# Optimization experiments

Hardware: AMD Instinct MI355X
Metric: run time of the kernel (lower is better)

The kernel has to match this reference:

```python
import jax, jax.numpy as jnp
import numpy as np

B, T, DIN, H, NOUT = 256, 512, 64, 512, 128


def setup_inputs() -> dict:
    key = jax.random.key(0)
    ks = jax.random.split(key, 11)
    s = 1.0 / np.sqrt(H)  # PyTorch GRU init scale
    inp = {"x": jax.random.normal(ks[0], (B, T, DIN), dtype=jnp.float32)}
    # layer 0 (input DIN), layer 1 (input H); gate order: r, z, n
    inp["w_ih0"] = jax.random.uniform(ks[1], (3 * H, DIN), minval=-s, maxval=s)
    inp["w_hh0"] = jax.random.uniform(ks[2], (3 * H, H), minval=-s, maxval=s)
    inp["b_ih0"] = jax.random.uniform(ks[3], (3 * H,), minval=-s, maxval=s)
    inp["b_hh0"] = jax.random.uniform(ks[4], (3 * H,), minval=-s, maxval=s)
    inp["w_ih1"] = jax.random.uniform(ks[5], (3 * H, H), minval=-s, maxval=s)
    inp["w_hh1"] = jax.random.uniform(ks[6], (3 * H, H), minval=-s, maxval=s)
    inp["b_ih1"] = jax.random.uniform(ks[7], (3 * H,), minval=-s, maxval=s)
    inp["b_hh1"] = jax.random.uniform(ks[8], (3 * H,), minval=-s, maxval=s)
    inp["w_fc"] = jax.random.uniform(ks[9], (NOUT, H), minval=-s, maxval=s)
    inp["b_fc"] = jax.random.uniform(ks[10], (NOUT,), minval=-s, maxval=s)
    return inp


def _gru_layer(x_seq, w_ih, w_hh, b_ih, b_hh):
    # x_seq: [B, T, Din] -> hidden trajectory [B, T, H]
    xg = jnp.einsum('btd,gd->btg', x_seq, w_ih) + b_ih  # [B, T, 3H], precomputed input gates
    h0 = jnp.zeros((x_seq.shape[0], w_hh.shape[1]), dtype=x_seq.dtype)

    def step(h, xg_t):
        hg = h @ w_hh.T + b_hh
        xr, xz, xn = jnp.split(xg_t, 3, axis=-1)
        hr, hz, hn = jnp.split(hg, 3, axis=-1)
        r = jax.nn.sigmoid(xr + hr)
        z = jax.nn.sigmoid(xz + hz)
        n = jnp.tanh(xn + r * hn)
        h_new = (1.0 - z) * n + z * h
        return h_new, h_new

    _, hs = jax.lax.scan(step, h0, jnp.swapaxes(xg, 0, 1))  # [T, B, H]
    return jnp.swapaxes(hs, 0, 1)


def reference(x, w_ih0, w_hh0, b_ih0, b_hh0, w_ih1, w_hh1, b_ih1, b_hh1, w_fc, b_fc):
    h1 = _gru_layer(x, w_ih0, w_hh0, b_ih0, b_hh0)   # [B, T, H]
    h2 = _gru_layer(h1, w_ih1, w_hh1, b_ih1, b_hh1)  # [B, T, H]
    last = h2[:, -1, :]                               # [B, H]
    return last @ w_fc.T + b_fc                       # [B, NOUT]
```

## Files before the change

kernel.cpp:

```cpp
#include <hip/hip_runtime.h>
#include <math.h>

typedef unsigned short u16;
typedef __attribute__((ext_vector_type(8))) short s8v;
typedef __attribute__((ext_vector_type(4))) float f4v;
typedef __attribute__((ext_vector_type(4))) int   i4v;

constexpr int kB    = 256;
constexpr int kT    = 512;
constexpr int kDIN  = 64;
constexpr int kH    = 512;
constexpr int kG3   = 1536;
constexpr int kNOUT = 128;
constexpr int kPlane = 8 * 2 * 16 * 512;

__device__ __forceinline__ u16 f2bf(float f) {
  union { float f; unsigned u; } v; v.f = f;
  unsigned r = (v.u + 0x7FFFu + ((v.u >> 16) & 1u)) >> 16;
  return (u16)r;
}
__device__ __forceinline__ float fsig(float x) {
  x = fminf(fmaxf(x, -30.f), 30.f);
  float e = __expf(-x);
  return __fdividef(1.f, 1.f + e);
}
__device__ __forceinline__ float ftanh(float x) {
  x = fminf(fmaxf(x, -15.f), 15.f);
  float e = __expf(-2.f * x);
  return __fdividef(1.f - e, 1.f + e);
}

__device__ __forceinline__ void load_afrag16(const u16* base, i4v a[16]) {
  asm volatile(
      "global_load_dwordx4 %0, %16, off sc0 sc1\n\t"
      "global_load_dwordx4 %1, %16, off offset:1024 sc0 sc1\n\t"
      "global_load_dwordx4 %2, %16, off offset:2048 sc0 sc1\n\t"
      "global_load_dwordx4 %3, %16, off offset:3072 sc0 sc1\n\t"
      "global_load_dwordx4 %4, %17, off sc0 sc1\n\t"
      "global_load_dwordx4 %5, %17, off offset:1024 sc0 sc1\n\t"
      "global_load_dwordx4 %6, %17, off offset:2048 sc0 sc1\n\t"
      "global_load_dwordx4 %7, %17, off offset:3072 sc0 sc1\n\t"
      "global_load_dwordx4 %8, %18, off sc0 sc1\n\t"
      "global_load_dwordx4 %9, %18, off offset:1024 sc0 sc1\n\t"
      "global_load_dwordx4 %10, %18, off offset:2048 sc0 sc1\n\t"
      "global_load_dwordx4 %11, %18, off offset:3072 sc0 sc1\n\t"
      "global_load_dwordx4 %12, %19, off sc0 sc1\n\t"
      "global_load_dwordx4 %13, %19, off offset:1024 sc0 sc1\n\t"
      "global_load_dwordx4 %14, %19, off offset:2048 sc0 sc1\n\t"
      "global_load_dwordx4 %15, %19, off offset:3072 sc0 sc1\n\t"
      "s_waitcnt vmcnt(0)"
      : "=&v"(a[0]), "=&v"(a[1]), "=&v"(a[2]), "=&v"(a[3]),
        "=&v"(a[4]), "=&v"(a[5]), "=&v"(a[6]), "=&v"(a[7]),
        "=&v"(a[8]), "=&v"(a[9]), "=&v"(a[10]), "=&v"(a[11]),
        "=&v"(a[12]), "=&v"(a[13]), "=&v"(a[14]), "=&v"(a[15])
      : "v"(base), "v"(base + 4 * 512), "v"(base + 8 * 512), "v"(base + 12 * 512)
      : "memory");
}

__device__ __forceinline__ void store_h_l0(
    u16* p0, u16* p1, u16* p2, u16* p3,
    u16* q0, u16* q1, u16* q2, u16* q3,
    unsigned v0, unsigned v1, unsigned v2, unsigned v3) {
  asm volatile(
      "global_store_short %0, %8, off sc0 sc1\n\t"
      "global_store_short %1, %9, off sc0 sc1\n\t"
      "global_store_short %2, %10, off sc0 sc1\n\t"
      "global_store_short %3, %11, off sc0 sc1\n\t"
      "global_store_short %4, %8, off\n\t"
      "global_store_short %5, %9, off\n\t"
      "global_store_short %6, %10, off\n\t"
      "global_store_short %7, %11, off\n\t"
      "s_waitcnt vmcnt(4)"
      :: "v"(p0), "v"(p1), "v"(p2), "v"(p3),
         "v"(q0), "v"(q1), "v"(q2), "v"(q3),
         "v"(v0), "v"(v1), "v"(v2), "v"(v3)
      : "memory");
}
__device__ __forceinline__ void store_h_l1(
    u16* p0, u16* p1, u16* p2, u16* p3,
    unsigned v0, unsigned v1, unsigned v2, unsigned v3) {
  asm volatile(
      "global_store_short %0, %4, off sc0 sc1\n\t"
      "global_store_short %1, %5, off sc0 sc1\n\t"
      "global_store_short %2, %6, off sc0 sc1\n\t"
      "global_store_short %3, %7, off sc0 sc1\n\t"
      "s_waitcnt vmcnt(0)"
      :: "v"(p0), "v"(p1), "v"(p2), "v"(p3),
         "v"(v0), "v"(v1), "v"(v2), "v"(v3)
      : "memory");
}

__global__ void build_wslab(const float* __restrict__ w, u16* __restrict__ d) {
  int idx  = blockIdx.x * 256 + threadIdx.x;
  int lane = idx & 63, fg = idx >> 6;
  int jt = fg / 96, f = fg % 96;
  int nt = f >> 4, kt = f & 15;
  int g = nt >> 1, u = nt & 1;
  int row = g * 512 + jt * 32 + u * 16 + (lane & 15);
  int k0  = kt * 32 + (lane >> 4) * 8;
  const float* src = w + (size_t)row * 512 + k0;
  u16* dst = d + ((size_t)fg) * 512 + lane * 8;
#pragma unroll
  for (int i = 0; i < 8; i++) dst[i] = f2bf(src[i]);
}

__global__ __launch_bounds__(256, 1)
void coop_rec(int c, int TC, int nc, unsigned bar_base16, unsigned* bar,
              const float* __restrict__ xg0, const float* __restrict__ xg1,
              const u16* __restrict__ wslab0, const u16* __restrict__ wslab1,
              const float* __restrict__ bhh0, const float* __restrict__ bhh1,
              u16* __restrict__ h1seq, u16* __restrict__ hbuf,
              float* __restrict__ carry) {
  const int bid   = blockIdx.x;
  const int layer = bid >> 7;
  const int lb    = bid & 127;
  const int jt    = lb & 15, bt = lb >> 4;
  const int cc    = (layer == 0) ? c : c - 1;
  const bool active = (cc >= 0 && cc < nc);

  unsigned* mybar = bar + (size_t)(layer * 8 + bt) * 64;

  if (!active) {
    if (threadIdx.x == 0)
      __hip_atomic_fetch_add(mybar, (unsigned)TC, __ATOMIC_RELAXED,
                             __HIP_MEMORY_SCOPE_AGENT);
    return;
  }

  const float* xg    = layer ? xg1 : xg0;
  const u16*  wslab  = layer ? wslab1 : wslab0;
  const float* bhh   = layer ? bhh1 : bhh0;
  float* mycarry = carry + (size_t)layer * kB * kH;

  const int tid  = threadIdx.x;
  const int wv   = tid >> 6, lane = tid & 63;
  const int mt   = wv >> 1, u = wv & 1;
  const int b0   = bt * 32;
  const int jl   = lane & 15;
  const int jg   = jt * 32 + u * 16 + jl;
  const int mrow = (lane >> 4) * 4;

  s8v bfr[3][16];
  {
    const u16* base = wslab + (size_t)jt * 96 * 512;
#pragma unroll
    for (int g = 0; g < 3; ++g)
#pragma unroll
      for (int kt = 0; kt < 16; ++kt)
        bfr[g][kt] = *(const s8v*)&base[(size_t)((g * 2 + u) * 16 + kt) * 512 + lane * 8];
  }
  const float bh_r = bhh[jg], bh_z = bhh[512 + jg], bh_n = bhh[1024 + jg];

  float hp[4];
#pragma unroll
  for (int r = 0; r < 4; ++r)
    hp[r] = mycarry[(size_t)(b0 + mt * 16 + mrow + r) * 512 + jg];

  const size_t cons_off = ((size_t)((bt * 2 + mt) * 16)) * 512 + lane * 8;
  const size_t prod_off = ((size_t)((bt * 2 + mt) * 16 + jt)) * 512 +
                          (size_t)(16 * (u * 2 + (jl >> 3))) * 8 + (jl & 7);
  const int bbase = b0 + mt * 16 + mrow;

  float xv0[4], xv1[4], xv2[4];
  auto prefetch_xg = [&](int tt) {
#pragma unroll
    for (int r = 0; r < 4; ++r) {
      const float* xp = xg + ((size_t)(bbase + r) * TC + tt) * kG3;
      xv0[r] = xp[jg]; xv1[r] = xp[512 + jg]; xv2[r] = xp[1024 + jg];
    }
  };
  prefetch_xg(0);

  for (int t = 0; t < TC; ++t) {
    if (tid == 0) {
      unsigned tgt = bar_base16 + 16u * (unsigned)t;
      int guard = 0;
      while (__hip_atomic_load(mybar, __ATOMIC_RELAXED,
                               __HIP_MEMORY_SCOPE_AGENT) < tgt
             && ++guard < (1 << 21)) {
        __builtin_amdgcn_s_sleep(1);
      }
    }
    __syncthreads();

    const u16* plane = hbuf + (size_t)(layer * 2 + (t & 1)) * kPlane;
    i4v a[16];
    load_afrag16(plane + cons_off, a);

    f4v acc0 = {0.f, 0.f, 0.f, 0.f}, acc1 = acc0, acc2 = acc0;
#pragma unroll
    for (int kt = 0; kt < 16; ++kt) {
      const s8v av = __builtin_bit_cast(s8v, a[kt]);
      acc0 = __builtin_amdgcn_mfma_f32_16x16x32_bf16(av, bfr[0][kt], acc0, 0, 0, 0);
      acc1 = __builtin_amdgcn_mfma_f32_16x16x32_bf16(av, bfr[1][kt], acc1, 0, 0, 0);
      acc2 = __builtin_amdgcn_mfma_f32_16x16x32_bf16(av, bfr[2][kt], acc2, 0, 0, 0);
    }

    unsigned hv[4];
#pragma unroll
    for (int r = 0; r < 4; ++r) {
      float rr = fsig(xv0[r] + acc0[r] + bh_r);
      float zz = fsig(xv1[r] + acc1[r] + bh_z);
      float nn = ftanh(xv2[r] + rr * (acc2[r] + bh_n));
      float hn = (1.f - zz) * nn + zz * hp[r];
      hp[r] = hn;
      hv[r] = f2bf(hn);
    }

    u16* pb = hbuf + (size_t)(layer * 2 + ((t + 1) & 1)) * kPlane + prod_off;
    if (layer == 0) {
      u16* q = h1seq + ((size_t)bbase * TC + t) * 512 + jg;
      store_h_l0(pb + (size_t)(mrow + 0) * 8, pb + (size_t)(mrow + 1) * 8,
                 pb + (size_t)(mrow + 2) * 8, pb + (size_t)(mrow + 3) * 8,
                 q, q + (size_t)TC * 512, q + 2 * (size_t)TC * 512,
                 q + 3 * (size_t)TC * 512,
                 hv[0], hv[1], hv[2], hv[3]);
    } else {
      store_h_l1(pb + (size_t)(mrow + 0) * 8, pb + (size_t)(mrow + 1) * 8,
                 pb + (size_t)(mrow + 2) * 8, pb + (size_t)(mrow + 3) * 8,
                 hv[0], hv[1], hv[2], hv[3]);
    }
    __syncthreads();
    if (tid == 0)
      __hip_atomic_fetch_add(mybar, 1u, __ATOMIC_RELAXED,
                             __HIP_MEMORY_SCOPE_AGENT);
    if (t + 1 < TC) prefetch_xg(t + 1);
  }

#pragma unroll
  for (int r = 0; r < 4; ++r)
    mycarry[(size_t)(bbase + r) * 512 + jg] = hp[r];
}

__device__ void gemm_role(int idx, int TC,
                          const float* __restrict__ Af, const u16* __restrict__ Ab,
                          int Abstride, int Atoff, int K,
                          const float* __restrict__ Bf, const float* __restrict__ bias,
                          float* __restrict__ C, char* smem) {
  u16* As = (u16*)smem;
  u16* Bs = As + 128 * 40;
  const int tid = threadIdx.x;
  const int mt = idx / 12, nt = idx % 12;
  const int m0 = mt * 128, n0 = nt * 128;
  const int w = tid >> 6, lane = tid & 63;
  const int wm = w & 1, wn = w >> 1;
  const int ra = tid >> 2, koff = (tid & 3) * 8;

  const int r = m0 + ra;
  const size_t aoff = ((size_t)(r / TC) * Abstride + Atoff + (r % TC)) * K;
  const float* arowF = Af ? Af + aoff : nullptr;
  const u16*  arowB = Ab ? Ab + aoff : nullptr;
  const float* browF = Bf + (size_t)(n0 + ra) * K;

  f4v acc[4][2];
#pragma unroll
  for (int i = 0; i < 4; i++)
#pragma unroll
    for (int jn = 0; jn < 2; jn++) acc[i][jn] = (f4v){0.f, 0.f, 0.f, 0.f};

  for (int k0 = 0; k0 < K; k0 += 32) {
    s8v av, bv;
    if (arowB) {
      av = *(const s8v*)(arowB + k0 + koff);
    } else {
      u16 tmp[8];
      const float* ap = arowF + k0 + koff;
#pragma unroll
      for (int i = 0; i < 8; i++) tmp[i] = f2bf(ap[i]);
      av = *(s8v*)tmp;
    }
    {
      u16 tmp[8];
      const float* bp = browF + k0 + koff;
#pragma unroll
      for (int i = 0; i < 8; i++) tmp[i] = f2bf(bp[i]);
      bv = *(s8v*)tmp;
    }
    __syncthreads();
    *(s8v*)&As[ra * 40 + koff] = av;
    *(s8v*)&Bs[ra * 40 + koff] = bv;
    __syncthreads();
    s8v af[4];
#pragma unroll
    for (int i = 0; i < 4; i++)
      af[i] = *(const s8v*)&As[(wm * 64 + i * 16 + (lane & 15)) * 40 + (lane >> 4) * 8];
#pragma unroll
    for (int jn = 0; jn < 2; jn++) {
      s8v bf = *(const s8v*)&Bs[(wn * 32 + jn * 16 + (lane & 15)) * 40 + (lane >> 4) * 8];
#pragma unroll
      for (int i = 0; i < 4; i++)
        acc[i][jn] = __builtin_amdgcn_mfma_f32_16x16x32_bf16(af[i], bf, acc[i][jn], 0, 0, 0);
    }
  }

#pragma unroll
  for (int jn = 0; jn < 2; jn++) {
    int n = n0 + wn * 32 + jn * 16 + (lane & 15);
    float bv2 = bias[n];
#pragma unroll
    for (int i = 0; i < 4; i++) {
      int mrow = m0 + wm * 64 + i * 16 + (lane >> 4) * 4;
#pragma unroll
      for (int reg = 0; reg < 4; reg++)
        C[(size_t)(mrow + reg) * kG3 + n] = acc[i][jn][reg] + bv2;
    }
  }
}

__global__ __launch_bounds__(512)
void gemm_kernel(int TC, const float* Af, const u16* Ab, int Abstride, int Atoff,
                 int K, const float* Bf, const float* bias, float* C) {
  __shared__ __align__(16) char smem[2 * 128 * 40 * 2];
  gemm_role(blockIdx.x, TC, Af, Ab, Abstride, Atoff, K, Bf, bias, C, smem);
}

__global__ __launch_bounds__(512)
void gemm2_kernel(int TC, int G1, int do0,
                  const float* x, int atoff0, const u16* h1seq,
                  const float* wih0, const float* bih0, float* xg0,
                  const float* wih1, const float* bih1, float* xg1) {
  __shared__ __align__(16) char smem[2 * 128 * 40 * 2];
  if ((int)blockIdx.x < G1) {
    gemm_role(blockIdx.x, TC, nullptr, h1seq, TC, 0, kH, wih1, bih1, xg1, smem);
  } else if (do0) {
    gemm_role(blockIdx.x - G1, TC, x, nullptr, kT, atoff0, kDIN, wih0, bih0,
              xg0, smem);
  }
}

__global__ __launch_bounds__(128)
void fc_kernel(const float* __restrict__ h, const float* __restrict__ wfc,
               const float* __restrict__ bfc, float* __restrict__ out) {
  const int b = blockIdx.x;
  const int n = threadIdx.x;
  const float* hrow = h + (size_t)b * kH;
  const float* wrow = wfc + (size_t)n * kH;
  float acc = 0.f;
#pragma unroll 4
  for (int k = 0; k < kH; k += 4) {
    const float4 hv = *(const float4*)&hrow[k];
    const float4 wv = *(const float4*)&wrow[k];
    acc = fmaf(hv.x, wv.x, acc); acc = fmaf(hv.y, wv.y, acc);
    acc = fmaf(hv.z, wv.z, acc); acc = fmaf(hv.w, wv.w, acc);
  }
  out[(size_t)b * kNOUT + n] = acc + bfc[n];
}

extern "C" void kernel_launch(void* const* d_in, const int* in_sizes, int n_in,
                              void* d_out, int out_size, void* d_ws, size_t ws_size,
                              hipStream_t stream) {
  const float* x     = (const float*)d_in[0];
  const float* w_ih0 = (const float*)d_in[1];
  const float* w_hh0 = (const float*)d_in[2];
  const float* b_ih0 = (const float*)d_in[3];
  const float* b_hh0 = (const float*)d_in[4];
  const float* w_ih1 = (const float*)d_in[5];
  const float* w_hh1 = (const float*)d_in[6];
  const float* b_ih1 = (const float*)d_in[7];
  const float* b_hh1 = (const float*)d_in[8];
  const float* w_fc  = (const float*)d_in[9];
  const float* b_fc  = (const float*)d_in[10];
  float* out = (float*)d_out;

  auto need = [](int tc) -> size_t {
    size_t s = 0;
    s += 2 * (size_t)kB * tc * kG3 * 4;
    s += (size_t)kB * tc * kH * 2;
    s += 2 * (size_t)kG3 * kH * 2;
    s += 4 * (size_t)kPlane * 2;
    s += 2 * (size_t)kB * kH * 4;
    s += 32768;
    return s;
  };
  int TC = 64;
  while (TC > 2 && need(TC) > ws_size) TC >>= 1;
  const int nc = kT / TC;

  char* p = (char*)d_ws;
  auto carve = [&](size_t bytes) {
    char* r = p; p += (bytes + 255) & ~(size_t)255; return r;
  };
  float* xg0   = (float*)carve((size_t)kB * TC * kG3 * 4);
  float* xg1   = (float*)carve((size_t)kB * TC * kG3 * 4);
  u16* h1seq   = (u16*)carve((size_t)kB * TC * kH * 2);
  u16* wslab0  = (u16*)carve((size_t)kG3 * kH * 2);
  u16* wslab1  = (u16*)carve((size_t)kG3 * kH * 2);
  u16* hbuf    = (u16*)carve(4 * (size_t)kPlane * 2);
  float* carry = (float*)carve(2 * (size_t)kB * kH * 4);
  unsigned* bar = (unsigned*)carve(32 * 64 * sizeof(unsigned));

  build_wslab<<<384, 256, 0, stream>>>(w_hh0, wslab0);
  build_wslab<<<384, 256, 0, stream>>>(w_hh1, wslab1);
  hipMemsetAsync(hbuf, 0, 4 * (size_t)kPlane * 2 + 2 * (size_t)kB * kH * 4, stream);
  hipMemsetAsync(bar, 0, 32 * 64 * sizeof(unsigned), stream);

  const int G1 = 24 * TC;

  gemm_kernel<<<dim3(G1), 512, 0, stream>>>(TC, x, nullptr, kT, 0, kDIN,
                                            w_ih0, b_ih0, xg0);

  for (int c = 0; c <= nc; ++c) {
    unsigned base16 = (unsigned)c * 16u * (unsigned)TC;
    coop_rec<<<dim3(256), dim3(256), 0, stream>>>(
        c, TC, nc, base16, bar, xg0, xg1, wslab0, wslab1,
        b_hh0, b_hh1, h1seq, hbuf, carry);
    if (c < nc) {
      int do0 = (c + 1 < nc) ? 1 : 0;
      gemm2_kernel<<<dim3(2 * G1), 512, 0, stream>>>(
          TC, G1, do0, x, (c + 1) * TC, h1seq,
          w_ih0, b_ih0, xg0, w_ih1, b_ih1, xg1);
    }
  }

  fc_kernel<<<dim3(kB), dim3(kNOUT), 0, stream>>>(
      carry + (size_t)kB * kH, w_fc, b_fc, out);
}
```

Before: 2.586 ms.

## Fuse input-gate GEMMs into recurrent kernel with double-buffered chunk pipeline

Merges the per-chunk input-projection GEMM launches into the recurrent kernel as extra blocks. It double-buffers xg and h1 so that layer-1 recurrence runs two chunks behind layer 0, and the GEMM for chunk c-1 (layer 1) and c+1 (layer 0) runs alongside the recurrence. The GEMM is reworked to 256 threads with a 4x4 MFMA tile per wave, and TC is halved to 32 so the double buffers fit. This aims to remove the serial gap between GEMM and recurrence launches. In exchange it adds more launches, one extra pipeline stage and contention between GEMM blocks and the persistent recurrent blocks.

```diff
diff --git a/kernel.cpp b/kernel.cpp
--- a/kernel.cpp
+++ b/kernel.cpp
@@ -104,18 +104,124 @@
   for (int i = 0; i < 8; i++) dst[i] = f2bf(src[i]);
 }
 
+__device__ void gemm_role256(int idx, int TC,
+                             const float* __restrict__ Af, const u16* __restrict__ Ab,
+                             int Abstride, int Atoff, int K,
+                             const float* __restrict__ Bf, const float* __restrict__ bias,
+                             float* __restrict__ C, char* smem) {
+  u16* As = (u16*)smem;
+  u16* Bs = As + 128 * 40;
+  const int tid = threadIdx.x;
+  const int mt = idx / 12, nt = idx % 12;
+  const int m0 = mt * 128, n0 = nt * 128;
+  const int w = tid >> 6, lane = tid & 63;
+  const int wm = w & 1, wn = w >> 1;
+  const int ra = tid >> 1, koff = (tid & 1) * 16;
+
+  const int r = m0 + ra;
+  const size_t aoff = ((size_t)(r / TC) * Abstride + Atoff + (r % TC)) * K;
+  const float* arowF = Af ? Af + aoff : nullptr;
+  const u16*  arowB = Ab ? Ab + aoff : nullptr;
+  const float* browF = Bf + (size_t)(n0 + ra) * K;
+
+  f4v acc[4][4];
+#pragma unroll
+  for (int i = 0; i < 4; i++)
+#pragma unroll
+    for (int j = 0; j < 4; j++) acc[i][j] = (f4v){0.f, 0.f, 0.f, 0.f};
+
+  for (int k0 = 0; k0 < K; k0 += 32) {
+    s8v av0, av1, bv0, bv1;
+    if (arowB) {
+      av0 = *(const s8v*)(arowB + k0 + koff);
+      av1 = *(const s8v*)(arowB + k0 + koff + 8);
+    } else {
+      u16 t0[8], t1[8];
+      const float* ap = arowF + k0 + koff;
+#pragma unroll
+      for (int i = 0; i < 8; i++) { t0[i] = f2bf(ap[i]); t1[i] = f2bf(ap[8 + i]); }
+      av0 = *(s8v*)t0; av1 = *(s8v*)t1;
+    }
+    {
+      u16 t0[8], t1[8];
+      const float* bp = browF + k0 + koff;
+#pragma unroll
+      for (int i = 0; i < 8; i++) { t0[i] = f2bf(bp[i]); t1[i] = f2bf(bp[8 + i]); }
+      bv0 = *(s8v*)t0; bv1 = *(s8v*)t1;
+    }
+    __syncthreads();
+    *(s8v*)&As[ra * 40 + koff]     = av0;
+    *(s8v*)&As[ra * 40 + koff + 8] = av1;
+    *(s8v*)&Bs[ra * 40 + koff]     = bv0;
+    *(s8v*)&Bs[ra * 40 + koff + 8] = bv1;
+    __syncthreads();
+    s8v af[4], bf[4];
+#pragma unroll
+    for (int i = 0; i < 4; i++)
+      af[i] = *(const s8v*)&As[(wm * 64 + i * 16 + (lane & 15)) * 40 + (lane >> 4) * 8];
+#pragma unroll
+    for (int j = 0; j < 4; j++)
+      bf[j] = *(const s8v*)&Bs[(wn * 64 + j * 16 + (lane & 15)) * 40 + (lane >> 4) * 8];
+#pragma unroll
+    for (int j = 0; j < 4; j++)
+#pragma unroll
+      for (int i = 0; i < 4; i++)
+        acc[i][j] = __builtin_amdgcn_mfma_f32_16x16x32_bf16(af[i], bf[j], acc[i][j], 0, 0, 0);
+  }
+
+#pragma unroll
+  for (int j = 0; j < 4; j++) {
+    int n = n0 + wn * 64 + j * 16 + (lane & 15);
+    float bv2 = bias[n];
+#pragma unroll
+    for (int i = 0; i < 4; i++) {
+      int mrow = m0 + wm * 64 + i * 16 + (lane >> 4) * 4;
+#pragma unroll
+      for (int reg = 0; reg < 4; reg++)
+        C[(size_t)(mrow + reg) * kG3 + n] = acc[i][j][reg] + bv2;
+    }
+  }
+}
+
 __global__ __launch_bounds__(256, 1)
-void coop_rec(int c, int TC, int nc, unsigned bar_base16, unsigned* bar,
-              const float* __restrict__ xg0, const float* __restrict__ xg1,
-              const u16* __restrict__ wslab0, const u16* __restrict__ wslab1,
-              const float* __restrict__ bhh0, const float* __restrict__ bhh1,
-              u16* __restrict__ h1seq, u16* __restrict__ hbuf,
-              float* __restrict__ carry) {
-  const int bid   = blockIdx.x;
+void fused_rec(int c, int TC, int nc, int G1, unsigned bar_base16,
+               unsigned* bar,
+               const float* __restrict__ x,
+               const float* __restrict__ xg0a, const float* __restrict__ xg0b,
+               const float* __restrict__ xg1a, const float* __restrict__ xg1b,
+               u16* __restrict__ h1a, u16* __restrict__ h1b,
+               const u16* __restrict__ wslab0, const u16* __restrict__ wslab1,
+               const float* __restrict__ bhh0, const float* __restrict__ bhh1,
+               const float* __restrict__ wih0, const float* __restrict__ bih0,
+               const float* __restrict__ wih1, const float* __restrict__ bih1,
+               u16* __restrict__ hbuf, float* __restrict__ carry) {
+  const int bid = blockIdx.x;
+
+  if (bid >= 256) {
+    __shared__ __align__(16) char smem[2 * 128 * 40 * 2];
+    int g = bid - 256;
+    if (g < G1) {
+      int cp = c - 1;
+      if (cp >= 0 && cp < nc) {
+        const u16* A = (cp & 1) ? h1b : h1a;
+        float* O = (float*)((cp & 1) ? xg1b : xg1a);
+        gemm_role256(g, TC, nullptr, A, TC, 0, kH, wih1, bih1, O, smem);
+      }
+    } else {
+      int cn = c + 1;
+      if (cn < nc) {
+        float* O = (float*)((cn & 1) ? xg0b : xg0a);
+        gemm_role256(g - G1, TC, x, nullptr, kT, cn * TC, kDIN, wih0, bih0,
+                     O, smem);
+      }
+    }
+    return;
+  }
+
   const int layer = bid >> 7;
   const int lb    = bid & 127;
   const int jt    = lb & 15, bt = lb >> 4;
-  const int cc    = (layer == 0) ? c : c - 1;
+  const int cc    = (layer == 0) ? c : c - 2;
   const bool active = (cc >= 0 && cc < nc);
 
   unsigned* mybar = bar + (size_t)(layer * 8 + bt) * 64;
@@ -127,9 +233,11 @@
     return;
   }
 
-  const float* xg    = layer ? xg1 : xg0;
-  const u16*  wslab  = layer ? wslab1 : wslab0;
-  const float* bhh   = layer ? bhh1 : bhh0;
+  const float* xg   = layer ? ((cc & 1) ? xg1b : xg1a)
+                            : ((cc & 1) ? xg0b : xg0a);
+  u16* h1seq        = (cc & 1) ? h1b : h1a;
+  const u16*  wslab = layer ? wslab1 : wslab0;
+  const float* bhh  = layer ? bhh1 : bhh0;
   float* mycarry = carry + (size_t)layer * kB * kH;
 
   const int tid  = threadIdx.x;
@@ -232,100 +340,12 @@
     mycarry[(size_t)(bbase + r) * 512 + jg] = hp[r];
 }
 
-__device__ void gemm_role(int idx, int TC,
-                          const float* __restrict__ Af, const u16* __restrict__ Ab,
-                          int Abstride, int Atoff, int K,
-                          const float* __restrict__ Bf, const float* __restrict__ bias,
-                          float* __restrict__ C, char* smem) {
-  u16* As = (u16*)smem;
-  u16* Bs = As + 128 * 40;
-  const int tid = threadIdx.x;
-  const int mt = idx / 12, nt = idx % 12;
-  const int m0 = mt * 128, n0 = nt * 128;
-  const int w = tid >> 6, lane = tid & 63;
-  const int wm = w & 1, wn = w >> 1;
-  const int ra = tid >> 2, koff = (tid & 3) * 8;
-
-  const int r = m0 + ra;
-  const size_t aoff = ((size_t)(r / TC) * Abstride + Atoff + (r % TC)) * K;
-  const float* arowF = Af ? Af + aoff : nullptr;
-  const u16*  arowB = Ab ? Ab + aoff : nullptr;
-  const float* browF = Bf + (size_t)(n0 + ra) * K;
-
-  f4v acc[4][2];
-#pragma unroll
-  for (int i = 0; i < 4; i++)
-#pragma unroll
-    for (int jn = 0; jn < 2; jn++) acc[i][jn] = (f4v){0.f, 0.f, 0.f, 0.f};
-
-  for (int k0 = 0; k0 < K; k0 += 32) {
-    s8v av, bv;
-    if (arowB) {
-      av = *(const s8v*)(arowB + k0 + koff);
-    } else {
-      u16 tmp[8];
-      const float* ap = arowF + k0 + koff;
-#pragma unroll
-      for (int i = 0; i < 8; i++) tmp[i] = f2bf(ap[i]);
-      av = *(s8v*)tmp;
-    }
-    {
-      u16 tmp[8];
-      const float* bp = browF + k0 + koff;
-#pragma unroll
-      for (int i = 0; i < 8; i++) tmp[i] = f2bf(bp[i]);
-      bv = *(s8v*)tmp;
-    }
-    __syncthreads();
-    *(s8v*)&As[ra * 40 + koff] = av;
-    *(s8v*)&Bs[ra * 40 + koff] = bv;
-    __syncthreads();
-    s8v af[4];
-#pragma unroll
-    for (int i = 0; i < 4; i++)
-      af[i] = *(const s8v*)&As[(wm * 64 + i * 16 + (lane & 15)) * 40 + (lane >> 4) * 8];
-#pragma unroll
-    for (int jn = 0; jn < 2; jn++) {
-      s8v bf = *(const s8v*)&Bs[(wn * 32 + jn * 16 + (lane & 15)) * 40 + (lane >> 4) * 8];
-#pragma unroll
-      for (int i = 0; i < 4; i++)
-        acc[i][jn] = __builtin_amdgcn_mfma_f32_16x16x32_bf16(af[i], bf, acc[i][jn], 0, 0, 0);
-    }
-  }
-
-#pragma unroll
-  for (int jn = 0; jn < 2; jn++) {
-    int n = n0 + wn * 32 + jn * 16 + (lane & 15);
-    float bv2 = bias[n];
-#pragma unroll
-    for (int i = 0; i < 4; i++) {
-      int mrow = m0 + wm * 64 + i * 16 + (lane >> 4) * 4;
-#pragma unroll
-      for (int reg = 0; reg < 4; reg++)
-        C[(size_t)(mrow + reg) * kG3 + n] = acc[i][jn][reg] + bv2;
-    }
-  }
-}
-
-__global__ __launch_bounds__(512)
-void gemm_kernel(int TC, const float* Af, const u16* Ab, int Abstride, int Atoff,
-                 int K, const float* Bf, const float* bias, float* C) {
+__global__ __launch_bounds__(256)
+void gemm_kernel256(int TC, const float* Af, const u16* Ab, int Abstride,
+                    int Atoff, int K, const float* Bf, const float* bias,
+                    float* C) {
   __shared__ __align__(16) char smem[2 * 128 * 40 * 2];
-  gemm_role(blockIdx.x, TC, Af, Ab, Abstride, Atoff, K, Bf, bias, C, smem);
-}
-
-__global__ __launch_bounds__(512)
-void gemm2_kernel(int TC, int G1, int do0,
-                  const float* x, int atoff0, const u16* h1seq,
-                  const float* wih0, const float* bih0, float* xg0,
-                  const float* wih1, const float* bih1, float* xg1) {
-  __shared__ __align__(16) char smem[2 * 128 * 40 * 2];
-  if ((int)blockIdx.x < G1) {
-    gemm_role(blockIdx.x, TC, nullptr, h1seq, TC, 0, kH, wih1, bih1, xg1, smem);
-  } else if (do0) {
-    gemm_role(blockIdx.x - G1, TC, x, nullptr, kT, atoff0, kDIN, wih0, bih0,
-              xg0, smem);
-  }
+  gemm_role256(blockIdx.x, TC, Af, Ab, Abstride, Atoff, K, Bf, bias, C, smem);
 }
 
 __global__ __launch_bounds__(128)
@@ -364,15 +384,15 @@
 
   auto need = [](int tc) -> size_t {
     size_t s = 0;
-    s += 2 * (size_t)kB * tc * kG3 * 4;
-    s += (size_t)kB * tc * kH * 2;
+    s += 4 * (size_t)kB * tc * kG3 * 4;
+    s += 2 * (size_t)kB * tc * kH * 2;
     s += 2 * (size_t)kG3 * kH * 2;
     s += 4 * (size_t)kPlane * 2;
     s += 2 * (size_t)kB * kH * 4;
-    s += 32768;
+    s += 65536;
     return s;
   };
-  int TC = 64;
+  int TC = 32;
   while (TC > 2 && need(TC) > ws_size) TC >>= 1;
   const int nc = kT / TC;
 
@@ -380,9 +400,12 @@
   auto carve = [&](size_t bytes) {
     char* r = p; p += (bytes + 255) & ~(size_t)255; return r;
   };
-  float* xg0   = (float*)carve((size_t)kB * TC * kG3 * 4);
-  float* xg1   = (float*)carve((size_t)kB * TC * kG3 * 4);
-  u16* h1seq   = (u16*)carve((size_t)kB * TC * kH * 2);
+  float* xg0a  = (float*)carve((size_t)kB * TC * kG3 * 4);
+  float* xg0b  = (float*)carve((size_t)kB * TC * kG3 * 4);
+  float* xg1a  = (float*)carve((size_t)kB * TC * kG3 * 4);
+  float* xg1b  = (float*)carve((size_t)kB * TC * kG3 * 4);
+  u16* h1a     = (u16*)carve((size_t)kB * TC * kH * 2);
+  u16* h1b     = (u16*)carve((size_t)kB * TC * kH * 2);
   u16* wslab0  = (u16*)carve((size_t)kG3 * kH * 2);
   u16* wslab1  = (u16*)carve((size_t)kG3 * kH * 2);
   u16* hbuf    = (u16*)carve(4 * (size_t)kPlane * 2);
@@ -396,20 +419,17 @@
 
   const int G1 = 24 * TC;
 
-  gemm_kernel<<<dim3(G1), 512, 0, stream>>>(TC, x, nullptr, kT, 0, kDIN,
-                                            w_ih0, b_ih0, xg0);
-
-  for (int c = 0; c <= nc; ++c) {
+  gemm_kernel256<<<dim3(G1), 256, 0, stream>>>(TC, x, nullptr, kT, 0, kDIN,
+                                               w_ih0, b_ih0, xg0a);
+
+  for (int c = 0; c <= nc + 1; ++c) {
     unsigned base16 = (unsigned)c * 16u * (unsigned)TC;
-    coop_rec<<<dim3(256), dim3(256), 0, stream>>>(
-        c, TC, nc, base16, bar, xg0, xg1, wslab0, wslab1,
-        b_hh0, b_hh1, h1seq, hbuf, carry);
-    if (c < nc) {
-      int do0 = (c + 1 < nc) ? 1 : 0;
-      gemm2_kernel<<<dim3(2 * G1), 512, 0, stream>>>(
-          TC, G1, do0, x, (c + 1) * TC, h1seq,
-          w_ih0, b_ih0, xg0, w_ih1, b_ih1, xg1);
-    }
+    fused_rec<<<dim3(256 + 2 * G1), dim3(256), 0, stream>>>(
+        c, TC, nc, G1, base16, bar, x,
+        xg0a, xg0b, xg1a, xg1b, h1a, h1b,
+        wslab0, wslab1, b_hh0, b_hh1,
+        w_ih0, b_ih0, w_ih1, b_ih1,
+        hbuf, carry);
   }
 
   fc_kernel<<<dim3(kB), dim3(kNOUT), 0, stream>>>(
```

New measurement: 3.066 ms. 1.19x slower.

## Fuse input projections into a single persistent wavefront-pipelined two-layer GRU kernel

Applied to the files above, without the earlier changes.

Removes the chunked launches of the recurrent kernel and the separate input-gate GEMM kernels. Both layers now run in one persistent kernel: layer 0 computes its input projection in-loop from a pre-packed bf16 x plane, and layer 1 computes its input projection from layer 0's live hidden state. Per-layer counters form a skewed wavefront so layer 1 runs one step behind layer 0. The goal is to drop the fp32 xg round trips through memory, the h1seq staging and the per-chunk launch and sync overhead. The cost is extra MFMA work in the serial step path, and layer 1 now streams its input weights from global memory every step.

```diff
diff --git a/kernel.cpp b/kernel.cpp
--- a/kernel.cpp
+++ b/kernel.cpp
@@ -13,6 +13,9 @@
 constexpr int kG3   = 1536;
 constexpr int kNOUT = 128;
 constexpr int kPlane = 8 * 2 * 16 * 512;
+constexpr int kXStep = 16 * 2 * 512;
+
+#define MFMA16 __builtin_amdgcn_mfma_f32_16x16x32_bf16
 
 __device__ __forceinline__ u16 f2bf(float f) {
   union { float f; unsigned u; } v; v.f = f;
@@ -56,27 +59,59 @@
       : "v"(base), "v"(base + 4 * 512), "v"(base + 8 * 512), "v"(base + 12 * 512)
       : "memory");
 }
-
-__device__ __forceinline__ void store_h_l0(
-    u16* p0, u16* p1, u16* p2, u16* p3,
-    u16* q0, u16* q1, u16* q2, u16* q3,
-    unsigned v0, unsigned v1, unsigned v2, unsigned v3) {
+__device__ __forceinline__ void load16_nw(const u16* base, i4v a[16]) {
   asm volatile(
-      "global_store_short %0, %8, off sc0 sc1\n\t"
-      "global_store_short %1, %9, off sc0 sc1\n\t"
-      "global_store_short %2, %10, off sc0 sc1\n\t"
-      "global_store_short %3, %11, off sc0 sc1\n\t"
-      "global_store_short %4, %8, off\n\t"
-      "global_store_short %5, %9, off\n\t"
-      "global_store_short %6, %10, off\n\t"
-      "global_store_short %7, %11, off\n\t"
-      "s_waitcnt vmcnt(4)"
-      :: "v"(p0), "v"(p1), "v"(p2), "v"(p3),
-         "v"(q0), "v"(q1), "v"(q2), "v"(q3),
-         "v"(v0), "v"(v1), "v"(v2), "v"(v3)
+      "global_load_dwordx4 %0, %16, off sc0 sc1\n\t"
+      "global_load_dwordx4 %1, %16, off offset:1024 sc0 sc1\n\t"
+      "global_load_dwordx4 %2, %16, off offset:2048 sc0 sc1\n\t"
+      "global_load_dwordx4 %3, %16, off offset:3072 sc0 sc1\n\t"
+      "global_load_dwordx4 %4, %17, off sc0 sc1\n\t"
+      "global_load_dwordx4 %5, %17, off offset:1024 sc0 sc1\n\t"
+      "global_load_dwordx4 %6, %17, off offset:2048 sc0 sc1\n\t"
+      "global_load_dwordx4 %7, %17, off offset:3072 sc0 sc1\n\t"
+      "global_load_dwordx4 %8, %18, off sc0 sc1\n\t"
+      "global_load_dwordx4 %9, %18, off offset:1024 sc0 sc1\n\t"
+      "global_load_dwordx4 %10, %18, off offset:2048 sc0 sc1\n\t"
+      "global_load_dwordx4 %11, %18, off offset:3072 sc0 sc1\n\t"
+      "global_load_dwordx4 %12, %19, off sc0 sc1\n\t"
+      "global_load_dwordx4 %13, %19, off offset:1024 sc0 sc1\n\t"
+      "global_load_dwordx4 %14, %19, off offset:2048 sc0 sc1\n\t"
+      "global_load_dwordx4 %15, %19, off offset:3072 sc0 sc1"
+      : "=&v"(a[0]), "=&v"(a[1]), "=&v"(a[2]), "=&v"(a[3]),
+        "=&v"(a[4]), "=&v"(a[5]), "=&v"(a[6]), "=&v"(a[7]),
+        "=&v"(a[8]), "=&v"(a[9]), "=&v"(a[10]), "=&v"(a[11]),
+        "=&v"(a[12]), "=&v"(a[13]), "=&v"(a[14]), "=&v"(a[15])
+      : "v"(base), "v"(base + 4 * 512), "v"(base + 8 * 512), "v"(base + 12 * 512)
       : "memory");
 }
-__device__ __forceinline__ void store_h_l1(
+__device__ __forceinline__ void load16_w16(const u16* base, i4v a[16]) {
+  asm volatile(
+      "global_load_dwordx4 %0, %16, off sc0 sc1\n\t"
+      "global_load_dwordx4 %1, %16, off offset:1024 sc0 sc1\n\t"
+      "global_load_dwordx4 %2, %16, off offset:2048 sc0 sc1\n\t"
+      "global_load_dwordx4 %3, %16, off offset:3072 sc0 sc1\n\t"
+      "global_load_dwordx4 %4, %17, off sc0 sc1\n\t"
+      "global_load_dwordx4 %5, %17, off offset:1024 sc0 sc1\n\t"
+      "global_load_dwordx4 %6, %17, off offset:2048 sc0 sc1\n\t"
+      "global_load_dwordx4 %7, %17, off offset:3072 sc0 sc1\n\t"
+      "global_load_dwordx4 %8, %18, off sc0 sc1\n\t"
+      "global_load_dwordx4 %9, %18, off offset:1024 sc0 sc1\n\t"
+      "global_load_dwordx4 %10, %18, off offset:2048 sc0 sc1\n\t"
+      "global_load_dwordx4 %11, %18, off offset:3072 sc0 sc1\n\t"
+      "global_load_dwordx4 %12, %19, off sc0 sc1\n\t"
+      "global_load_dwordx4 %13, %19, off offset:1024 sc0 sc1\n\t"
+      "global_load_dwordx4 %14, %19, off offset:2048 sc0 sc1\n\t"
+      "global_load_dwordx4 %15, %19, off offset:3072 sc0 sc1\n\t"
+      "s_waitcnt vmcnt(16)"
+      : "=&v"(a[0]), "=&v"(a[1]), "=&v"(a[2]), "=&v"(a[3]),
+        "=&v"(a[4]), "=&v"(a[5]), "=&v"(a[6]), "=&v"(a[7]),
+        "=&v"(a[8]), "=&v"(a[9]), "=&v"(a[10]), "=&v"(a[11]),
+        "=&v"(a[12]), "=&v"(a[13]), "=&v"(a[14]), "=&v"(a[15])
+      : "v"(base), "v"(base + 4 * 512), "v"(base + 8 * 512), "v"(base + 12 * 512)
+      : "memory");
+}
+
+__device__ __forceinline__ void store_h4(
     u16* p0, u16* p1, u16* p2, u16* p3,
     unsigned v0, unsigned v1, unsigned v2, unsigned v3) {
   asm volatile(
@@ -90,6 +125,13 @@
       : "memory");
 }
 
+__device__ __forceinline__ void wait_ge(unsigned* p, unsigned tgt) {
+  int guard = 0;
+  while (__hip_atomic_load(p, __ATOMIC_RELAXED, __HIP_MEMORY_SCOPE_AGENT) < tgt
+         && ++guard < (1 << 22))
+    __builtin_amdgcn_s_sleep(1);
+}
+
 __global__ void build_wslab(const float* __restrict__ w, u16* __restrict__ d) {
   int idx  = blockIdx.x * 256 + threadIdx.x;
   int lane = idx & 63, fg = idx >> 6;
@@ -104,227 +146,214 @@
   for (int i = 0; i < 8; i++) dst[i] = f2bf(src[i]);
 }
 
+__global__ void build_wslab_ih0(const float* __restrict__ w, u16* __restrict__ d) {
+  int idx  = blockIdx.x * 256 + threadIdx.x;
+  int lane = idx & 63, fg = idx >> 6;
+  int jt = fg / 12, f = fg % 12;
+  int nt = f >> 1, kt = f & 1;
+  int g = nt >> 1, u = nt & 1;
+  int row = g * 512 + jt * 32 + u * 16 + (lane & 15);
+  int k0  = kt * 32 + (lane >> 4) * 8;
+  const float* src = w + (size_t)row * kDIN + k0;
+  u16* dst = d + ((size_t)fg) * 512 + lane * 8;
+#pragma unroll
+  for (int i = 0; i < 8; i++) dst[i] = f2bf(src[i]);
+}
+
+__global__ void build_xplane(const float* __restrict__ x, u16* __restrict__ d) {
+  int idx  = blockIdx.x * 256 + threadIdx.x;
+  int lane = idx & 63, fg = idx >> 6;
+  int kt = fg & 1, m = (fg >> 1) & 15, T = fg >> 5;
+  int b  = m * 16 + (lane & 15);
+  int k0 = kt * 32 + (lane >> 4) * 8;
+  const float* src = x + ((size_t)b * kT + T) * kDIN + k0;
+  u16* dst = d + ((size_t)fg) * 512 + lane * 8;
+#pragma unroll
+  for (int i = 0; i < 8; i++) dst[i] = f2bf(src[i]);
+}
+
 __global__ __launch_bounds__(256, 1)
-void coop_rec(int c, int TC, int nc, unsigned bar_base16, unsigned* bar,
-              const float* __restrict__ xg0, const float* __restrict__ xg1,
-              const u16* __restrict__ wslab0, const u16* __restrict__ wslab1,
-              const float* __restrict__ bhh0, const float* __restrict__ bhh1,
-              u16* __restrict__ h1seq, u16* __restrict__ hbuf,
-              float* __restrict__ carry) {
+void rec_all(unsigned* bar, const u16* __restrict__ xpl,
+             const u16* __restrict__ slab0hh, const u16* __restrict__ slab0ih,
+             const u16* __restrict__ slab1hh, const u16* __restrict__ slab1ih,
+             const float* __restrict__ bih0, const float* __restrict__ bhh0,
+             const float* __restrict__ bih1, const float* __restrict__ bhh1,
+             u16* __restrict__ hbuf, float* __restrict__ carry) {
   const int bid   = blockIdx.x;
   const int layer = bid >> 7;
   const int lb    = bid & 127;
   const int jt    = lb & 15, bt = lb >> 4;
-  const int cc    = (layer == 0) ? c : c - 1;
-  const bool active = (cc >= 0 && cc < nc);
-
-  unsigned* mybar = bar + (size_t)(layer * 8 + bt) * 64;
-
-  if (!active) {
-    if (threadIdx.x == 0)
-      __hip_atomic_fetch_add(mybar, (unsigned)TC, __ATOMIC_RELAXED,
-                             __HIP_MEMORY_SCOPE_AGENT);
-    return;
-  }
-
-  const float* xg    = layer ? xg1 : xg0;
-  const u16*  wslab  = layer ? wslab1 : wslab0;
-  const float* bhh   = layer ? bhh1 : bhh0;
-  float* mycarry = carry + (size_t)layer * kB * kH;
-
-  const int tid  = threadIdx.x;
-  const int wv   = tid >> 6, lane = tid & 63;
-  const int mt   = wv >> 1, u = wv & 1;
-  const int b0   = bt * 32;
-  const int jl   = lane & 15;
-  const int jg   = jt * 32 + u * 16 + jl;
-  const int mrow = (lane >> 4) * 4;
-
-  s8v bfr[3][16];
-  {
-    const u16* base = wslab + (size_t)jt * 96 * 512;
-#pragma unroll
-    for (int g = 0; g < 3; ++g)
-#pragma unroll
-      for (int kt = 0; kt < 16; ++kt)
-        bfr[g][kt] = *(const s8v*)&base[(size_t)((g * 2 + u) * 16 + kt) * 512 + lane * 8];
-  }
-  const float bh_r = bhh[jg], bh_z = bhh[512 + jg], bh_n = bhh[1024 + jg];
-
-  float hp[4];
-#pragma unroll
-  for (int r = 0; r < 4; ++r)
-    hp[r] = mycarry[(size_t)(b0 + mt * 16 + mrow + r) * 512 + jg];
+  const int tid   = threadIdx.x;
+  const int wv    = tid >> 6, lane = tid & 63;
+  const int mt    = wv >> 1, u = wv & 1;
+  const int jl    = lane & 15;
+  const int jg    = jt * 32 + u * 16 + jl;
+  const int mrow  = (lane >> 4) * 4;
+  const int bbase = bt * 32 + mt * 16 + mrow;
+
+  unsigned* barL0 = bar + (size_t)bt * 64;
+  unsigned* barL1 = bar + (size_t)(8 + bt) * 64;
 
   const size_t cons_off = ((size_t)((bt * 2 + mt) * 16)) * 512 + lane * 8;
   const size_t prod_off = ((size_t)((bt * 2 + mt) * 16 + jt)) * 512 +
                           (size_t)(16 * (u * 2 + (jl >> 3))) * 8 + (jl & 7);
-  const int bbase = b0 + mt * 16 + mrow;
-
-  float xv0[4], xv1[4], xv2[4];
-  auto prefetch_xg = [&](int tt) {
-#pragma unroll
-    for (int r = 0; r < 4; ++r) {
-      const float* xp = xg + ((size_t)(bbase + r) * TC + tt) * kG3;
-      xv0[r] = xp[jg]; xv1[r] = xp[512 + jg]; xv2[r] = xp[1024 + jg];
+
+  if (layer == 0) {
+    s8v bh[3][16];
+    {
+      const u16* base = slab0hh + (size_t)jt * 96 * 512 + (size_t)lane * 8;
+#pragma unroll
+      for (int g = 0; g < 3; ++g)
+#pragma unroll
+        for (int kt = 0; kt < 16; ++kt)
+          bh[g][kt] = *(const s8v*)(base + (size_t)((g * 2 + u) * 16 + kt) * 512);
     }
-  };
-  prefetch_xg(0);
-
-  for (int t = 0; t < TC; ++t) {
-    if (tid == 0) {
-      unsigned tgt = bar_base16 + 16u * (unsigned)t;
-      int guard = 0;
-      while (__hip_atomic_load(mybar, __ATOMIC_RELAXED,
-                               __HIP_MEMORY_SCOPE_AGENT) < tgt
-             && ++guard < (1 << 21)) {
-        __builtin_amdgcn_s_sleep(1);
-      }
+    s8v bx[3][2];
+    {
+      const u16* base = slab0ih + (size_t)jt * 12 * 512 + (size_t)lane * 8;
+#pragma unroll
+      for (int g = 0; g < 3; ++g)
+#pragma unroll
+        for (int kt = 0; kt < 2; ++kt)
+          bx[g][kt] = *(const s8v*)(base + (size_t)((g * 2 + u) * 2 + kt) * 512);
     }
-    __syncthreads();
-
-    const u16* plane = hbuf + (size_t)(layer * 2 + (t & 1)) * kPlane;
-    i4v a[16];
-    load_afrag16(plane + cons_off, a);
-
-    f4v acc0 = {0.f, 0.f, 0.f, 0.f}, acc1 = acc0, acc2 = acc0;
-#pragma unroll
-    for (int kt = 0; kt < 16; ++kt) {
-      const s8v av = __builtin_bit_cast(s8v, a[kt]);
-      acc0 = __builtin_amdgcn_mfma_f32_16x16x32_bf16(av, bfr[0][kt], acc0, 0, 0, 0);
-      acc1 = __builtin_amdgcn_mfma_f32_16x16x32_bf16(av, bfr[1][kt], acc1, 0, 0, 0);
-      acc2 = __builtin_amdgcn_mfma_f32_16x16x32_bf16(av, bfr[2][kt], acc2, 0, 0, 0);
+    const float br  = bih0[jg] + bhh0[jg];
+    const float bz  = bih0[512 + jg] + bhh0[512 + jg];
+    const float bni = bih0[1024 + jg], bnh = bhh0[1024 + jg];
+    float hp[4] = {0.f, 0.f, 0.f, 0.f};
+
+    const size_t xoff = (size_t)((bt * 2 + mt) * 2) * 512 + (size_t)lane * 8;
+    s8v ax0 = *(const s8v*)(xpl + xoff);
+    s8v ax1 = *(const s8v*)(xpl + xoff + 512);
+
+    for (int t = 0; t < kT; ++t) {
+      if (tid == 0) {
+        if (t) wait_ge(barL0, 16u * (unsigned)t);
+      } else if (tid == 64) {
+        if (t >= 2) wait_ge(barL1, 16u * (unsigned)(t - 1));
+      }
+      __syncthreads();
+
+      i4v a[16];
+      load_afrag16(hbuf + (size_t)(t & 1) * kPlane + cons_off, a);
+
+      const f4v z4 = {0.f, 0.f, 0.f, 0.f};
+      f4v acc0, acc1, acc2, acc2x;
+      acc0  = MFMA16(ax0, bx[0][0], z4, 0, 0, 0);
+      acc0  = MFMA16(ax1, bx[0][1], acc0, 0, 0, 0);
+      acc1  = MFMA16(ax0, bx[1][0], z4, 0, 0, 0);
+      acc1  = MFMA16(ax1, bx[1][1], acc1, 0, 0, 0);
+      acc2x = MFMA16(ax0, bx[2][0], z4, 0, 0, 0);
+      acc2x = MFMA16(ax1, bx[2][1], acc2x, 0, 0, 0);
+      acc2  = z4;
+#pragma unroll
+      for (int kt = 0; kt < 16; ++kt) {
+        const s8v av = __builtin_bit_cast(s8v, a[kt]);
+        acc0 = MFMA16(av, bh[0][kt], acc0, 0, 0, 0);
+        acc1 = MFMA16(av, bh[1][kt], acc1, 0, 0, 0);
+        acc2 = MFMA16(av, bh[2][kt], acc2, 0, 0, 0);
+      }
+
+      unsigned hv[4];
+#pragma unroll
+      for (int r = 0; r < 4; ++r) {
+        float rr = fsig(acc0[r] + br);
+        float zz = fsig(acc1[r] + bz);
+        float nn = ftanh(acc2x[r] + bni + rr * (acc2[r] + bnh));
+        float hn = (1.f - zz) * nn + zz * hp[r];
+        hp[r] = hn;
+        hv[r] = f2bf(hn);
+      }
+
+      u16* pb = hbuf + (size_t)((t + 1) & 1) * kPlane + prod_off;
+      store_h4(pb + (size_t)(mrow + 0) * 8, pb + (size_t)(mrow + 1) * 8,
+               pb + (size_t)(mrow + 2) * 8, pb + (size_t)(mrow + 3) * 8,
+               hv[0], hv[1], hv[2], hv[3]);
+      __syncthreads();
+      if (tid == 0)
+        __hip_atomic_fetch_add(barL0, 1u, __ATOMIC_RELAXED,
+                               __HIP_MEMORY_SCOPE_AGENT);
+      if (t + 1 < kT) {
+        const u16* xb = xpl + (size_t)(t + 1) * kXStep + xoff;
+        ax0 = *(const s8v*)xb;
+        ax1 = *(const s8v*)(xb + 512);
+      }
     }
-
-    unsigned hv[4];
-#pragma unroll
-    for (int r = 0; r < 4; ++r) {
-      float rr = fsig(xv0[r] + acc0[r] + bh_r);
-      float zz = fsig(xv1[r] + acc1[r] + bh_z);
-      float nn = ftanh(xv2[r] + rr * (acc2[r] + bh_n));
-      float hn = (1.f - zz) * nn + zz * hp[r];
-      hp[r] = hn;
-      hv[r] = f2bf(hn);
+  } else {
+    s8v bh[3][16];
+    {
+      const u16* base = slab1hh + (size_t)jt * 96 * 512 + (size_t)lane * 8;
+#pragma unroll
+      for (int g = 0; g < 3; ++g)
+#pragma unroll
+        for (int kt = 0; kt < 16; ++kt)
+          bh[g][kt] = *(const s8v*)(base + (size_t)((g * 2 + u) * 16 + kt) * 512);
     }
-
-    u16* pb = hbuf + (size_t)(layer * 2 + ((t + 1) & 1)) * kPlane + prod_off;
-    if (layer == 0) {
-      u16* q = h1seq + ((size_t)bbase * TC + t) * 512 + jg;
-      store_h_l0(pb + (size_t)(mrow + 0) * 8, pb + (size_t)(mrow + 1) * 8,
-                 pb + (size_t)(mrow + 2) * 8, pb + (size_t)(mrow + 3) * 8,
-                 q, q + (size_t)TC * 512, q + 2 * (size_t)TC * 512,
-                 q + 3 * (size_t)TC * 512,
-                 hv[0], hv[1], hv[2], hv[3]);
-    } else {
-      store_h_l1(pb + (size_t)(mrow + 0) * 8, pb + (size_t)(mrow + 1) * 8,
-                 pb + (size_t)(mrow + 2) * 8, pb + (size_t)(mrow + 3) * 8,
-                 hv[0], hv[1], hv[2], hv[3]);
+    const u16* wbase = slab1ih + (size_t)jt * 96 * 512 + (size_t)lane * 8;
+    const float br  = bih1[jg] + bhh1[jg];
+    const float bz  = bih1[512 + jg] + bhh1[512 + jg];
+    const float bni = bih1[1024 + jg], bnh = bhh1[1024 + jg];
+    float hp[4] = {0.f, 0.f, 0.f, 0.f};
+
+    for (int t = 0; t < kT; ++t) {
+      if (tid == 0) {
+        wait_ge(barL0, 16u * (unsigned)(t + 1));
+      } else if (tid == 64) {
+        if (t) wait_ge(barL1, 16u * (unsigned)t);
+      }
+      __syncthreads();
+
+      i4v a[16], a2[16];
+      load16_nw(hbuf + (size_t)((t + 1) & 1) * kPlane + cons_off, a);
+      load16_w16(hbuf + (size_t)(2 + (t & 1)) * kPlane + cons_off, a2);
+      __builtin_amdgcn_sched_barrier(0);
+
+      const f4v z4 = {0.f, 0.f, 0.f, 0.f};
+      f4v acc0 = z4, acc1 = z4, acc2 = z4, acc2x = z4;
+#pragma unroll 4
+      for (int kt = 0; kt < 16; ++kt) {
+        s8v b0 = *(const s8v*)(wbase + (size_t)((0 + u) * 16 + kt) * 512);
+        s8v b1 = *(const s8v*)(wbase + (size_t)((2 + u) * 16 + kt) * 512);
+        s8v b2 = *(const s8v*)(wbase + (size_t)((4 + u) * 16 + kt) * 512);
+        const s8v av = __builtin_bit_cast(s8v, a[kt]);
+        acc0  = MFMA16(av, b0, acc0, 0, 0, 0);
+        acc1  = MFMA16(av, b1, acc1, 0, 0, 0);
+        acc2x = MFMA16(av, b2, acc2x, 0, 0, 0);
+      }
+      asm volatile("s_waitcnt vmcnt(0)" ::: "memory");
+      __builtin_amdgcn_sched_barrier(0);
+#pragma unroll
+      for (int kt = 0; kt < 16; ++kt) {
+        const s8v av = __builtin_bit_cast(s8v, a2[kt]);
+        acc0 = MFMA16(av, bh[0][kt], acc0, 0, 0, 0);
+        acc1 = MFMA16(av, bh[1][kt], acc1, 0, 0, 0);
+        acc2 = MFMA16(av, bh[2][kt], acc2, 0, 0, 0);
+      }
+
+      unsigned hv[4];
+#pragma unroll
+      for (int r = 0; r < 4; ++r) {
+        float rr = fsig(acc0[r] + br);
+        float zz = fsig(acc1[r] + bz);
+        float nn = ftanh(acc2x[r] + bni + rr * (acc2[r] + bnh));
+        float hn = (1.f - zz) * nn + zz * hp[r];
+        hp[r] = hn;
+        hv[r] = f2bf(hn);
+      }
+
+      u16* pb = hbuf + (size_t)(2 + ((t + 1) & 1)) * kPlane + prod_off;
+      store_h4(pb + (size_t)(mrow + 0) * 8, pb + (size_t)(mrow + 1) * 8,
+               pb + (size_t)(mrow + 2) * 8, pb + (size_t)(mrow + 3) * 8,
+               hv[0], hv[1], hv[2], hv[3]);
+      __syncthreads();
+      if (tid == 0)
+        __hip_atomic_fetch_add(barL1, 1u, __ATOMIC_RELAXED,
+                               __HIP_MEMORY_SCOPE_AGENT);
     }
-    __syncthreads();
-    if (tid == 0)
-      __hip_atomic_fetch_add(mybar, 1u, __ATOMIC_RELAXED,
-                             __HIP_MEMORY_SCOPE_AGENT);
-    if (t + 1 < TC) prefetch_xg(t + 1);
-  }
-
-#pragma unroll
-  for (int r = 0; r < 4; ++r)
-    mycarry[(size_t)(bbase + r) * 512 + jg] = hp[r];
-}
-
-__device__ void gemm_role(int idx, int TC,
-                          const float* __restrict__ Af, const u16* __restrict__ Ab,
-                          int Abstride, int Atoff, int K,
-                          const float* __restrict__ Bf, const float* __restrict__ bias,
-                          float* __restrict__ C, char* smem) {
-  u16* As = (u16*)smem;
-  u16* Bs = As + 128 * 40;
-  const int tid = threadIdx.x;
-  const int mt = idx / 12, nt = idx % 12;
-  const int m0 = mt * 128, n0 = nt * 128;
-  const int w = tid >> 6, lane = tid & 63;
-  const int wm = w & 1, wn = w >> 1;
-  const int ra = tid >> 2, koff = (tid & 3) * 8;
-
-  const int r = m0 + ra;
-  const size_t aoff = ((size_t)(r / TC) * Abstride + Atoff + (r % TC)) * K;
-  const float* arowF = Af ? Af + aoff : nullptr;
-  const u16*  arowB = Ab ? Ab + aoff : nullptr;
-  const float* browF = Bf + (size_t)(n0 + ra) * K;
-
-  f4v acc[4][2];
-#pragma unroll
-  for (int i = 0; i < 4; i++)
-#pragma unroll
-    for (int jn = 0; jn < 2; jn++) acc[i][jn] = (f4v){0.f, 0.f, 0.f, 0.f};
-
-  for (int k0 = 0; k0 < K; k0 += 32) {
-    s8v av, bv;
-    if (arowB) {
-      av = *(const s8v*)(arowB + k0 + koff);
-    } else {
-      u16 tmp[8];
-      const float* ap = arowF + k0 + koff;
-#pragma unroll
-      for (int i = 0; i < 8; i++) tmp[i] = f2bf(ap[i]);
-      av = *(s8v*)tmp;
-    }
-    {
-      u16 tmp[8];
-      const float* bp = browF + k0 + koff;
-#pragma unroll
-      for (int i = 0; i < 8; i++) tmp[i] = f2bf(bp[i]);
-      bv = *(s8v*)tmp;
-    }
-    __syncthreads();
-    *(s8v*)&As[ra * 40 + koff] = av;
-    *(s8v*)&Bs[ra * 40 + koff] = bv;
-    __syncthreads();
-    s8v af[4];
-#pragma unroll
-    for (int i = 0; i < 4; i++)
-      af[i] = *(const s8v*)&As[(wm * 64 + i * 16 + (lane & 15)) * 40 + (lane >> 4) * 8];
-#pragma unroll
-    for (int jn = 0; jn < 2; jn++) {
-      s8v bf = *(const s8v*)&Bs[(wn * 32 + jn * 16 + (lane & 15)) * 40 + (lane >> 4) * 8];
-#pragma unroll
-      for (int i = 0; i < 4; i++)
-        acc[i][jn] = __builtin_amdgcn_mfma_f32_16x16x32_bf16(af[i], bf, acc[i][jn], 0, 0, 0);
-    }
-  }
-
-#pragma unroll
-  for (int jn = 0; jn < 2; jn++) {
-    int n = n0 + wn * 32 + jn * 16 + (lane & 15);
-    float bv2 = bias[n];
-#pragma unroll
-    for (int i = 0; i < 4; i++) {
-      int mrow = m0 + wm * 64 + i * 16 + (lane >> 4) * 4;
-#pragma unroll
-      for (int reg = 0; reg < 4; reg++)
-        C[(size_t)(mrow + reg) * kG3 + n] = acc[i][jn][reg] + bv2;
-    }
-  }
-}
-
-__global__ __launch_bounds__(512)
-void gemm_kernel(int TC, const float* Af, const u16* Ab, int Abstride, int Atoff,
-                 int K, const float* Bf, const float* bias, float* C) {
-  __shared__ __align__(16) char smem[2 * 128 * 40 * 2];
-  gemm_role(blockIdx.x, TC, Af, Ab, Abstride, Atoff, K, Bf, bias, C, smem);
-}
-
-__global__ __launch_bounds__(512)
-void gemm2_kernel(int TC, int G1, int do0,
-                  const float* x, int atoff0, const u16* h1seq,
-                  const float* wih0, const float* bih0, float* xg0,
-                  const float* wih1, const float* bih1, float* xg1) {
-  __shared__ __align__(16) char smem[2 * 128 * 40 * 2];
-  if ((int)blockIdx.x < G1) {
-    gemm_role(blockIdx.x, TC, nullptr, h1seq, TC, 0, kH, wih1, bih1, xg1, smem);
-  } else if (do0) {
-    gemm_role(blockIdx.x - G1, TC, x, nullptr, kT, atoff0, kDIN, wih0, bih0,
-              xg0, smem);
+
+#pragma unroll
+    for (int r = 0; r < 4; ++r)
+      carry[(size_t)(bbase + r) * 512 + jg] = hp[r];
   }
 }
 
@@ -362,56 +391,30 @@
   const float* b_fc  = (const float*)d_in[10];
   float* out = (float*)d_out;
 
-  auto need = [](int tc) -> size_t {
-    size_t s = 0;
-    s += 2 * (size_t)kB * tc * kG3 * 4;
-    s += (size_t)kB * tc * kH * 2;
-    s += 2 * (size_t)kG3 * kH * 2;
-    s += 4 * (size_t)kPlane * 2;
-    s += 2 * (size_t)kB * kH * 4;
-    s += 32768;
-    return s;
-  };
-  int TC = 64;
-  while (TC > 2 && need(TC) > ws_size) TC >>= 1;
-  const int nc = kT / TC;
-
   char* p = (char*)d_ws;
   auto carve = [&](size_t bytes) {
     char* r = p; p += (bytes + 255) & ~(size_t)255; return r;
   };
-  float* xg0   = (float*)carve((size_t)kB * TC * kG3 * 4);
-  float* xg1   = (float*)carve((size_t)kB * TC * kG3 * 4);
-  u16* h1seq   = (u16*)carve((size_t)kB * TC * kH * 2);
-  u16* wslab0  = (u16*)carve((size_t)kG3 * kH * 2);
-  u16* wslab1  = (u16*)carve((size_t)kG3 * kH * 2);
+  u16* slab0hh = (u16*)carve((size_t)kG3 * kH * 2);
+  u16* slab1hh = (u16*)carve((size_t)kG3 * kH * 2);
+  u16* slab1ih = (u16*)carve((size_t)kG3 * kH * 2);
+  u16* slab0ih = (u16*)carve((size_t)kG3 * kDIN * 2);
+  u16* xpl     = (u16*)carve((size_t)kT * kXStep * 2);
   u16* hbuf    = (u16*)carve(4 * (size_t)kPlane * 2);
-  float* carry = (float*)carve(2 * (size_t)kB * kH * 4);
-  unsigned* bar = (unsigned*)carve(32 * 64 * sizeof(unsigned));
-
-  build_wslab<<<384, 256, 0, stream>>>(w_hh0, wslab0);
-  build_wslab<<<384, 256, 0, stream>>>(w_hh1, wslab1);
-  hipMemsetAsync(hbuf, 0, 4 * (size_t)kPlane * 2 + 2 * (size_t)kB * kH * 4, stream);
-  hipMemsetAsync(bar, 0, 32 * 64 * sizeof(unsigned), stream);
-
-  const int G1 = 24 * TC;
-
-  gemm_kernel<<<dim3(G1), 512, 0, stream>>>(TC, x, nullptr, kT, 0, kDIN,
-                                            w_ih0, b_ih0, xg0);
-
-  for (int c = 0; c <= nc; ++c) {
-    unsigned base16 = (unsigned)c * 16u * (unsigned)TC;
-    coop_rec<<<dim3(256), dim3(256), 0, stream>>>(
-        c, TC, nc, base16, bar, xg0, xg1, wslab0, wslab1,
-        b_hh0, b_hh1, h1seq, hbuf, carry);
-    if (c < nc) {
-      int do0 = (c + 1 < nc) ? 1 : 0;
-      gemm2_kernel<<<dim3(2 * G1), 512, 0, stream>>>(
-          TC, G1, do0, x, (c + 1) * TC, h1seq,
-          w_ih0, b_ih0, xg0, w_ih1, b_ih1, xg1);
-    }
-  }
-
-  fc_kernel<<<dim3(kB), dim3(kNOUT), 0, stream>>>(
-      carry + (size_t)kB * kH, w_fc, b_fc, out);
-}
+  float* carry = (float*)carve((size_t)kB * kH * 4);
+  unsigned* bar = (unsigned*)carve(16 * 64 * sizeof(unsigned));
+
+  build_wslab<<<384, 256, 0, stream>>>(w_hh0, slab0hh);
+  build_wslab<<<384, 256, 0, stream>>>(w_hh1, slab1hh);
+  build_wslab<<<384, 256, 0, stream>>>(w_ih1, slab1ih);
+  build_wslab_ih0<<<48, 256, 0, stream>>>(w_ih0, slab0ih);
+  build_xplane<<<4096, 256, 0, stream>>>(x, xpl);
+  hipMemsetAsync(hbuf, 0, 4 * (size_t)kPlane * 2, stream);
+  hipMemsetAsync(bar, 0, 16 * 64 * sizeof(unsigned), stream);
+
+  rec_all<<<dim3(256), dim3(256), 0, stream>>>(
+      bar, xpl, slab0hh, slab0ih, slab1hh, slab1ih,
+      b_ih0, b_hh0, b_ih1, b_hh1, hbuf, carry);
+
+  fc_kernel<<<dim3(kB), dim3(kNOUT), 0, stream>>>(carry, w_fc, b_fc, out);
+}
```

Measured after the change: 7.308 ms. +182.6%, slower.
